# Kernel optimization log

Hardware: AMD Instinct MI355X
Metric: run time of the kernel (lower is better)

## Reference

```python
import jax, jax.numpy as jnp
import numpy as np

OBJ = 6
N_OBJS = 16
ACT = 32
HID = 128


def _mlp(x, W1, b1, W2, b2, W3, b3):
    # RoboticsMLP with layer_sizes=[128,128]: Linear->ReLU->Linear->ReLU->Linear
    h = jax.nn.relu(x @ W1 + b1)
    h = jax.nn.relu(h @ W2 + b2)
    return h @ W3 + b3


def setup_inputs() -> dict:
    key = jax.random.key(0)
    ks = jax.random.split(key, 16)
    B = 4096
    s = lambda fan_in: 1.0 / np.sqrt(fan_in)
    u_in = OBJ + ACT          # 38
    b_in = 2 * OBJ + ACT      # 44
    return {
        "config": jax.random.normal(ks[0], (B, N_OBJS * OBJ), dtype=jnp.float32),
        "action": jax.random.normal(ks[1], (B, ACT), dtype=jnp.float32),
        "uW1": jax.random.normal(ks[2], (u_in, HID), dtype=jnp.float32) * s(u_in),
        "ub1": jnp.zeros((HID,), jnp.float32),
        "uW2": jax.random.normal(ks[3], (HID, HID), dtype=jnp.float32) * s(HID),
        "ub2": jnp.zeros((HID,), jnp.float32),
        "uW3": jax.random.normal(ks[4], (HID, OBJ), dtype=jnp.float32) * s(HID),
        "ub3": jnp.zeros((OBJ,), jnp.float32),
        "bW1": jax.random.normal(ks[5], (b_in, HID), dtype=jnp.float32) * s(b_in),
        "bb1": jnp.zeros((HID,), jnp.float32),
        "bW2": jax.random.normal(ks[6], (HID, HID), dtype=jnp.float32) * s(HID),
        "bb2": jnp.zeros((HID,), jnp.float32),
        "bW3": jax.random.normal(ks[7], (HID, OBJ), dtype=jnp.float32) * s(HID),
        "bb3": jnp.zeros((OBJ,), jnp.float32),
    }


def reference(config, action, uW1, ub1, uW2, ub2, uW3, ub3,
              bW1, bb1, bW2, bb2, bW3, bb3):
    B = config.shape[0]
    objs = config.reshape(B, N_OBJS, OBJ)                       # [B, N, 6]

    # Unary: per-object MLP on [obj, action]
    act_b = jnp.broadcast_to(action[:, None, :], (B, N_OBJS, ACT))
    u_in = jnp.concatenate([objs, act_b], axis=-1)              # [B, N, 6+A]
    u_out = _mlp(u_in, uW1, ub1, uW2, ub2, uW3, ub3)            # [B, N, 6]

    # Binary: all ordered pairs (i, j), i != j: [obj_i, obj_j, action]
    oi = jnp.broadcast_to(objs[:, :, None, :], (B, N_OBJS, N_OBJS, OBJ))
    oj = jnp.broadcast_to(objs[:, None, :, :], (B, N_OBJS, N_OBJS, OBJ))
    act_p = jnp.broadcast_to(action[:, None, None, :], (B, N_OBJS, N_OBJS, ACT))
    b_in = jnp.concatenate([oi, oj, act_p], axis=-1)            # [B, N, N, 12+A]
    b_out = _mlp(b_in, bW1, bb1, bW2, bb2, bW3, bb3)            # [B, N, N, 6]

    # zero out diagonal (i == j skipped in original) then sum over j
    mask = (1.0 - jnp.eye(N_OBJS, dtype=b_out.dtype))[None, :, :, None]
    b_sum = (b_out * mask).sum(axis=2)                          # [B, N, 6]

    out = objs + u_out + b_sum
    return out.reshape(B, N_OBJS * OBJ)
```

## Files before the change

kernel.cpp:

```cpp
#include <hip/hip_runtime.h>

typedef short bf16x8 __attribute__((ext_vector_type(8)));
typedef short bf16x4 __attribute__((ext_vector_type(4)));
typedef float f32x4 __attribute__((ext_vector_type(4)));

__device__ __forceinline__ unsigned short f2bf(float f) {
    unsigned int u = __float_as_uint(f);
    unsigned int r = u + 0x7FFFu + ((u >> 16) & 1u);
    return (unsigned short)(r >> 16);
}

__device__ __forceinline__ unsigned pkbf(float a, float b) {
    unsigned r;
    asm volatile("v_cvt_pk_bf16_f32 %0, %1, %2" : "=v"(r) : "v"(a), "v"(b));
    return r;
}

__device__ __forceinline__ f32x4 mfma16(bf16x4 a, bf16x4 b, f32x4 c) {
#if __has_builtin(__builtin_amdgcn_mfma_f32_16x16x16bf16_1k)
    return __builtin_amdgcn_mfma_f32_16x16x16bf16_1k(a, b, c, 0, 0, 0);
#elif __has_builtin(__builtin_amdgcn_mfma_f32_16x16x16_bf16)
    return __builtin_amdgcn_mfma_f32_16x16x16_bf16(a, b, c, 0, 0, 0);
#else
    asm volatile("v_mfma_f32_16x16x16_bf16 %0, %1, %2, %0" : "+v"(c) : "v"(a), "v"(b));
    return c;
#endif
}

__global__ __launch_bounds__(256) void prep_all(
        const float* __restrict__ uW1, const float* __restrict__ uW2, const float* __restrict__ uW3,
        const float* __restrict__ bW1, const float* __restrict__ bW2, const float* __restrict__ bW3,
        unsigned short* __restrict__ ws) {
    int idx = blockIdx.x * 256 + threadIdx.x;
    if (idx >= 53248) {
        if (idx < 55296) {
            int li = idx - 53248;
            int e = li & 3, l = (li >> 2) & 63, s = li >> 8;
            int k = 16 * s + 4 * (l >> 4) + e, n = l & 15;
            float v = (n < 6) ? bW3[k * 6 + n] : 0.f;
            ws[53248 + li] = f2bf(v);
        }
        return;
    }
    const float* W; int Ksrc, Nsrc, ntsh; unsigned short* dst; int li;
    if (idx < 8192)       { W = uW1; Ksrc = 38;  Nsrc = 128; ntsh = 10; dst = ws;         li = idx; }
    else if (idx < 16384) { W = bW1; Ksrc = 44;  Nsrc = 128; ntsh = 10; dst = ws + 8192;  li = idx - 8192; }
    else if (idx < 32768) { W = uW2; Ksrc = 128; Nsrc = 128; ntsh = 11; dst = ws + 16384; li = idx - 16384; }
    else if (idx < 49152) { W = bW2; Ksrc = 128; Nsrc = 128; ntsh = 11; dst = ws + 32768; li = idx - 32768; }
    else if (idx < 51200) { W = uW3; Ksrc = 128; Nsrc = 6;   ntsh = 11; dst = ws + 49152; li = idx - 49152; }
    else                  { W = bW3; Ksrc = 128; Nsrc = 6;   ntsh = 11; dst = ws + 51200; li = idx - 51200; }
    int e  = li & 7;
    int l  = (li >> 3) & 63;
    int KS = (ntsh == 10) ? 2 : 4;
    int ks = (li >> 9) & (KS - 1);
    int nt = li >> ntsh;
    int k  = ks * 32 + (l >> 4) * 8 + e;
    int n  = nt * 16 + (l & 15);
    float v = (k < Ksrc && n < Nsrc) ? W[k * Nsrc + n] : 0.0f;
    dst[li] = f2bf(v);
}

__global__ __launch_bounds__(256, 3) void unary_kernel(
        const float* __restrict__ config, const float* __restrict__ action,
        const unsigned short* __restrict__ W1f, const float* __restrict__ b1,
        const unsigned short* __restrict__ W2f, const float* __restrict__ b2,
        const unsigned short* __restrict__ W3f, const float* __restrict__ b3,
        float* __restrict__ out) {
    __shared__ __align__(16) unsigned char smem[4 * 8192];
    const int tid = threadIdx.x;
    const int w = tid >> 6;
    const int l = tid & 63;
    const int g = l >> 4;
    const int c = l & 15;
    unsigned char* buf = smem + w * 8192;

    {
        const int rowL = l >> 1;
        const int kh   = l & 1;
        const int sw   = (rowL & 7) << 4;
        const int base = rowL * 128 + kh * 64;
        const int rg = blockIdx.x * 128 + w * 32 + rowL;
        const int b = rg >> 4;
        const int i = rg & 15;
        const float* cbr = config + b * 96 + i * 6;
        const float* ab  = action + b * 32;
        if (kh == 0) {
            float ov[6];
            { const float2 t0 = *(const float2*)(cbr);
              const float2 t1 = *(const float2*)(cbr + 2);
              const float2 t2 = *(const float2*)(cbr + 4);
              ov[0]=t0.x; ov[1]=t0.y; ov[2]=t1.x; ov[3]=t1.y; ov[4]=t2.x; ov[5]=t2.y; }
            float av[26];
            #pragma unroll
            for (int q = 0; q < 6; ++q) {
                const float4 t = *(const float4*)(ab + 4 * q);
                av[4*q]=t.x; av[4*q+1]=t.y; av[4*q+2]=t.z; av[4*q+3]=t.w;
            }
            { const float2 t = *(const float2*)(ab + 24); av[24]=t.x; av[25]=t.y; }
            #pragma unroll
            for (int ch = 0; ch < 4; ++ch) {
                float x[8];
                #pragma unroll
                for (int t8 = 0; t8 < 8; ++t8) {
                    const int k = ch * 8 + t8;
                    x[t8] = (k < 6) ? ov[k] : av[k - 6];
                }
                union { unsigned uu[4]; bf16x8 v; } U;
                U.uu[0] = pkbf(x[0], x[1]); U.uu[1] = pkbf(x[2], x[3]);
                U.uu[2] = pkbf(x[4], x[5]); U.uu[3] = pkbf(x[6], x[7]);
                *(bf16x8*)(buf + ((base + ch * 16) ^ sw)) = U.v;
            }
        } else {
            float av2[6];
            { const float2 t = *(const float2*)(ab + 26); av2[0]=t.x; av2[1]=t.y; }
            { const float4 t = *(const float4*)(ab + 28); av2[2]=t.x; av2[3]=t.y; av2[4]=t.z; av2[5]=t.w; }
            {
                union { unsigned uu[4]; bf16x8 v; } U;
                U.uu[0] = pkbf(av2[0], av2[1]); U.uu[1] = pkbf(av2[2], av2[3]);
                U.uu[2] = pkbf(av2[4], av2[5]); U.uu[3] = 0u;
                *(bf16x8*)(buf + ((base + 0) ^ sw)) = U.v;
            }
            const bf16x8 z = {0,0,0,0,0,0,0,0};
            *(bf16x8*)(buf + ((base + 16) ^ sw)) = z;
            *(bf16x8*)(buf + ((base + 32) ^ sw)) = z;
            *(bf16x8*)(buf + ((base + 48) ^ sw)) = z;
        }
    }
    __syncthreads();

    const f32x4 zero4 = {0.f, 0.f, 0.f, 0.f};

    bf16x8 xf[2][2];
    #pragma unroll
    for (int mt = 0; mt < 2; ++mt)
        #pragma unroll
        for (int ks = 0; ks < 2; ++ks) {
            const int row = mt * 16 + c;
            xf[mt][ks] = *(const bf16x8*)(buf + ((row * 128 + ks * 64 + g * 16) ^ ((c & 7) << 4)));
        }

    #pragma unroll
    for (int nh = 0; nh < 2; ++nh) {
        f32x4 acc[2][4];
        #pragma unroll
        for (int mt = 0; mt < 2; ++mt)
            #pragma unroll
            for (int ntl = 0; ntl < 4; ++ntl) acc[mt][ntl] = zero4;
        #pragma unroll
        for (int ntl = 0; ntl < 4; ++ntl) {
            const int nt = nh * 4 + ntl;
            #pragma unroll
            for (int ks = 0; ks < 2; ++ks) {
                const bf16x8 bfr = *(const bf16x8*)(W1f + ((nt * 2 + ks) * 64 + l) * 8);
                #pragma unroll
                for (int mt = 0; mt < 2; ++mt)
                    acc[mt][ntl] = __builtin_amdgcn_mfma_f32_16x16x32_bf16(xf[mt][ks], bfr, acc[mt][ntl], 0, 0, 0);
            }
        }
        #pragma unroll
        for (int ntl = 0; ntl < 4; ++ntl) {
            const int col = (nh * 4 + ntl) * 16 + c;
            const float bias = b1[col];
            #pragma unroll
            for (int mt = 0; mt < 2; ++mt)
                #pragma unroll
                for (int r = 0; r < 4; ++r) {
                    const int row = mt * 16 + g * 4 + r;
                    const float hv = fmaxf(acc[mt][ntl][r] + bias, 0.f);
                    *(unsigned short*)(buf + ((row * 256 + col * 2) ^ ((row & 7) << 4))) = f2bf(hv);
                }
        }
    }
    __syncthreads();

    bf16x8 hf[2][4];
    #pragma unroll
    for (int mt = 0; mt < 2; ++mt)
        #pragma unroll
        for (int ks = 0; ks < 4; ++ks) {
            const int row = mt * 16 + c;
            hf[mt][ks] = *(const bf16x8*)(buf + ((row * 256 + ks * 64 + g * 16) ^ ((c & 7) << 4)));
        }

    #pragma unroll
    for (int nh = 0; nh < 2; ++nh) {
        f32x4 acc[2][4];
        #pragma unroll
        for (int mt = 0; mt < 2; ++mt)
            #pragma unroll
            for (int ntl = 0; ntl < 4; ++ntl) acc[mt][ntl] = zero4;
        #pragma unroll
        for (int ntl = 0; ntl < 4; ++ntl) {
            const int nt = nh * 4 + ntl;
            #pragma unroll
            for (int ks = 0; ks < 4; ++ks) {
                const bf16x8 bfr = *(const bf16x8*)(W2f + ((nt * 4 + ks) * 64 + l) * 8);
                #pragma unroll
                for (int mt = 0; mt < 2; ++mt)
                    acc[mt][ntl] = __builtin_amdgcn_mfma_f32_16x16x32_bf16(hf[mt][ks], bfr, acc[mt][ntl], 0, 0, 0);
            }
        }
        #pragma unroll
        for (int ntl = 0; ntl < 4; ++ntl) {
            const int col = (nh * 4 + ntl) * 16 + c;
            const float bias = b2[col];
            #pragma unroll
            for (int mt = 0; mt < 2; ++mt)
                #pragma unroll
                for (int r = 0; r < 4; ++r) {
                    const int row = mt * 16 + g * 4 + r;
                    const float hv = fmaxf(acc[mt][ntl][r] + bias, 0.f);
                    *(unsigned short*)(buf + ((row * 256 + col * 2) ^ ((row & 7) << 4))) = f2bf(hv);
                }
        }
    }
    __syncthreads();

    bf16x8 h2f[2][4];
    #pragma unroll
    for (int mt = 0; mt < 2; ++mt)
        #pragma unroll
        for (int ks = 0; ks < 4; ++ks) {
            const int row = mt * 16 + c;
            h2f[mt][ks] = *(const bf16x8*)(buf + ((row * 256 + ks * 64 + g * 16) ^ ((c & 7) << 4)));
        }

    f32x4 acc3[2];
    acc3[0] = zero4; acc3[1] = zero4;
    #pragma unroll
    for (int ks = 0; ks < 4; ++ks) {
        const bf16x8 bfr = *(const bf16x8*)(W3f + (ks * 64 + l) * 8);
        #pragma unroll
        for (int mt = 0; mt < 2; ++mt)
            acc3[mt] = __builtin_amdgcn_mfma_f32_16x16x32_bf16(h2f[mt][ks], bfr, acc3[mt], 0, 0, 0);
    }

    const int rgbase = blockIdx.x * 128 + w * 32;
    const float b3v = (c < 6) ? b3[c] : 0.f;
    #pragma unroll
    for (int mt = 0; mt < 2; ++mt)
        #pragma unroll
        for (int r = 0; r < 4; ++r) {
            const int rg = rgbase + mt * 16 + g * 4 + r;
            const int b = rg >> 4, i = rg & 15;
            if (c < 6) {
                const int idx = b * 96 + i * 6 + c;
                out[idx] = acc3[mt][r] + b3v + config[idx];
            }
        }
}

__global__ __launch_bounds__(256, 4) void binary_kernel(
        const float* __restrict__ config, const float* __restrict__ action,
        const unsigned short* __restrict__ W1f, const float* __restrict__ b1,
        const unsigned short* __restrict__ W2f, const float* __restrict__ b2,
        const unsigned short* __restrict__ W3s, const float* __restrict__ b3,
        float* __restrict__ out) {
    __shared__ __align__(16) unsigned char PQs[12288];

    const int tid = threadIdx.x;
    const int w = tid >> 6, l = tid & 63, g = l >> 4, c = l & 15;
    const int b = blockIdx.x >> 1, h = blockIdx.x & 1;
    const float* cb = config + b * 96;
    const float* ab = action + b * 32;
    const f32x4 zero4 = {0.f, 0.f, 0.f, 0.f};

    bf16x8 wf1[2][2];
    #pragma unroll
    for (int mt1 = 0; mt1 < 2; ++mt1)
        #pragma unroll
        for (int ksp = 0; ksp < 2; ++ksp)
            wf1[mt1][ksp] = *(const bf16x8*)(W1f + (((2 * w + mt1) * 2 + ksp) * 64 + l) * 8);
    f32x4 b1v[2];
    b1v[0] = *(const f32x4*)(b1 + 32 * w + 4 * g);
    b1v[1] = *(const f32x4*)(b1 + 32 * w + 16 + 4 * g);
    const float b3v = (c < 6) ? b3[c] : 0.f;

    bf16x8 tP0, tP1, tQ0;
    {
        const bf16x8 z8 = {0,0,0,0,0,0,0,0};
        tP0 = z8; tP1 = z8; tQ0 = z8;
        union { unsigned u[4]; bf16x8 v; } U;
        if (g == 0) {
            const float* obp = cb + (8 * h + (c & 7)) * 6;
            const float2 a0 = *(const float2*)obp, a1 = *(const float2*)(obp + 2), a2v = *(const float2*)(obp + 4);
            U.u[0] = pkbf(a0.x, a0.y); U.u[1] = pkbf(a1.x, a1.y); U.u[2] = pkbf(a2v.x, a2v.y); U.u[3] = 0u;
            tP0 = U.v;
            const float4 b0 = *(const float4*)(ab + 20), b1q = *(const float4*)(ab + 24);
            U.u[0] = pkbf(b0.x, b0.y); U.u[1] = pkbf(b0.z, b0.w);
            U.u[2] = pkbf(b1q.x, b1q.y); U.u[3] = pkbf(b1q.z, b1q.w);
            tP1 = U.v;
            const float2 q0 = *(const float2*)(cb + c * 6);
            U.u[0] = 0u; U.u[1] = 0u; U.u[2] = 0u; U.u[3] = pkbf(q0.x, q0.y);
            tQ0 = U.v;
        } else if (g == 1) {
            const float4 b0 = *(const float4*)(ab + 0);
            U.u[0] = 0u; U.u[1] = 0u; U.u[2] = pkbf(b0.x, b0.y); U.u[3] = pkbf(b0.z, b0.w);
            tP0 = U.v;
            const float4 b1q = *(const float4*)(ab + 28);
            U.u[0] = pkbf(b1q.x, b1q.y); U.u[1] = pkbf(b1q.z, b1q.w); U.u[2] = 0u; U.u[3] = 0u;
            tP1 = U.v;
            const float* obq = cb + c * 6;
            const float2 q1 = *(const float2*)(obq + 2), q2 = *(const float2*)(obq + 4);
            U.u[0] = pkbf(q1.x, q1.y); U.u[1] = pkbf(q2.x, q2.y); U.u[2] = 0u; U.u[3] = 0u;
            tQ0 = U.v;
        } else if (g == 2) {
            const float4 b0 = *(const float4*)(ab + 4), b1q = *(const float4*)(ab + 8);
            U.u[0] = pkbf(b0.x, b0.y); U.u[1] = pkbf(b0.z, b0.w);
            U.u[2] = pkbf(b1q.x, b1q.y); U.u[3] = pkbf(b1q.z, b1q.w);
            tP0 = U.v;
        } else {
            const float4 b0 = *(const float4*)(ab + 12), b1q = *(const float4*)(ab + 16);
            U.u[0] = pkbf(b0.x, b0.y); U.u[1] = pkbf(b0.z, b0.w);
            U.u[2] = pkbf(b1q.x, b1q.y); U.u[3] = pkbf(b1q.z, b1q.w);
            tP0 = U.v;
        }
    }

    {
        f32x4 acc1[2][2];
        acc1[0][0] = b1v[0]; acc1[0][1] = zero4;
        acc1[1][0] = b1v[1]; acc1[1][1] = zero4;
        #pragma unroll
        for (int mt1 = 0; mt1 < 2; ++mt1) {
            acc1[mt1][0] = __builtin_amdgcn_mfma_f32_16x16x32_bf16(wf1[mt1][0], tP0, acc1[mt1][0], 0, 0, 0);
            acc1[mt1][0] = __builtin_amdgcn_mfma_f32_16x16x32_bf16(wf1[mt1][1], tP1, acc1[mt1][0], 0, 0, 0);
            acc1[mt1][1] = __builtin_amdgcn_mfma_f32_16x16x32_bf16(wf1[mt1][0], tQ0, acc1[mt1][1], 0, 0, 0);
        }
        #pragma unroll
        for (int mt1 = 0; mt1 < 2; ++mt1) {
            const int fb = (32 * w + 16 * mt1 + 4 * g) * 4;
            if (c < 8) {
                float2 v0; v0.x = acc1[mt1][0][0]; v0.y = acc1[mt1][0][1];
                float2 v1; v1.x = acc1[mt1][0][2]; v1.y = acc1[mt1][0][3];
                *(float2*)(PQs + ((c * 512 + fb)     ^ ((c & 7) << 4))) = v0;
                *(float2*)(PQs + ((c * 512 + fb + 8) ^ ((c & 7) << 4))) = v1;
            }
            {
                const int row = 8 + c;
                float2 v0; v0.x = acc1[mt1][1][0]; v0.y = acc1[mt1][1][1];
                float2 v1; v1.x = acc1[mt1][1][2]; v1.y = acc1[mt1][1][3];
                *(float2*)(PQs + ((row * 512 + fb)     ^ ((c & 7) << 4))) = v0;
                *(float2*)(PQs + ((row * 512 + fb + 8) ^ ((c & 7) << 4))) = v1;
            }
        }
    }
    __syncthreads();

    const int i0 = h * 8 + 2 * w;
    bf16x8 h1f[2][4];
    #pragma unroll
    for (int ks = 0; ks < 4; ++ks) {
        const int kb = (32 * ks + 8 * g) * 4;
        const f32x4 q0 = *(const f32x4*)(PQs + (((8 + c) * 512 + kb) ^ ((c & 7) << 4)));
        const f32x4 q1 = *(const f32x4*)(PQs + (((8 + c) * 512 + kb + 16) ^ ((c & 7) << 4)));
        #pragma unroll
        for (int nt = 0; nt < 2; ++nt) {
            const int ip = 2 * w + nt;
            const f32x4 p0 = *(const f32x4*)(PQs + ((ip * 512 + kb) ^ ((ip & 7) << 4)));
            const f32x4 p1 = *(const f32x4*)(PQs + ((ip * 512 + kb + 16) ^ ((ip & 7) << 4)));
            union { unsigned u[4]; bf16x8 v; } un;
            un.u[0] = pkbf(fmaxf(p0[0] + q0[0], 0.f), fmaxf(p0[1] + q0[1], 0.f));
            un.u[1] = pkbf(fmaxf(p0[2] + q0[2], 0.f), fmaxf(p0[3] + q0[3], 0.f));
            un.u[2] = pkbf(fmaxf(p1[0] + q1[0], 0.f), fmaxf(p1[1] + q1[1], 0.f));
            un.u[3] = pkbf(fmaxf(p1[2] + q1[2], 0.f), fmaxf(p1[3] + q1[3], 0.f));
            h1f[nt][ks] = un.v;
        }
    }

    f32x4 acc3[2];
    acc3[0][0] = b3v; acc3[0][1] = b3v; acc3[0][2] = b3v; acc3[0][3] = b3v;
    acc3[1] = acc3[0];
    #pragma unroll
    for (int ks = 0; ks < 4; ++ks) {
        bf16x8 wfa[8];
        #pragma unroll
        for (int q = 0; q < 8; ++q)
            wfa[q] = *(const bf16x8*)(W2f + (((2 * ks + (q >> 2)) * 4 + (q & 3)) * 64 + l) * 8);
        union { uint2 u2; bf16x4 v; } w3b[2];
        w3b[0].u2 = *(const uint2*)(W3s + ((2 * ks)     * 64 + l) * 4);
        w3b[1].u2 = *(const uint2*)(W3s + ((2 * ks + 1) * 64 + l) * 4);
        const f32x4 bv0 = *(const f32x4*)(b2 + 32 * ks + 4 * g);
        const f32x4 bv1 = *(const f32x4*)(b2 + 32 * ks + 16 + 4 * g);
        __builtin_amdgcn_sched_barrier(0);

        f32x4 a2[2][2];
        a2[0][0] = bv0; a2[0][1] = bv0;
        a2[1][0] = bv1; a2[1][1] = bv1;
        #pragma unroll
        for (int ksp = 0; ksp < 4; ++ksp) {
            #pragma unroll
            for (int mt1 = 0; mt1 < 2; ++mt1) {
                a2[mt1][0] = __builtin_amdgcn_mfma_f32_16x16x32_bf16(wfa[mt1 * 4 + ksp], h1f[0][ksp], a2[mt1][0], 0, 0, 0);
                a2[mt1][1] = __builtin_amdgcn_mfma_f32_16x16x32_bf16(wfa[mt1 * 4 + ksp], h1f[1][ksp], a2[mt1][1], 0, 0, 0);
            }
        }
        #pragma unroll
        for (int mt1 = 0; mt1 < 2; ++mt1) {
            #pragma unroll
            for (int nt = 0; nt < 2; ++nt) {
                union { unsigned u[2]; bf16x4 v; } pa;
                pa.u[0] = pkbf(fmaxf(a2[mt1][nt][0], 0.f), fmaxf(a2[mt1][nt][1], 0.f));
                pa.u[1] = pkbf(fmaxf(a2[mt1][nt][2], 0.f), fmaxf(a2[mt1][nt][3], 0.f));
                acc3[nt] = mfma16(pa.v, w3b[mt1].v, acc3[nt]);
            }
        }
    }

    #pragma unroll
    for (int nt = 0; nt < 2; ++nt) {
        const int i = i0 + nt;
        float s = 0.f;
        #pragma unroll
        for (int r = 0; r < 4; ++r) {
            const int j = 4 * g + r;
            if (j != i) s += acc3[nt][r];
        }
        s += __shfl_xor(s, 16, 64);
        s += __shfl_xor(s, 32, 64);
        if (g == 0 && c < 6) out[b * 96 + i * 6 + c] += s;
    }
}

extern "C" void kernel_launch(void* const* d_in, const int* in_sizes, int n_in,
                              void* d_out, int out_size, void* d_ws, size_t ws_size,
                              hipStream_t stream) {
    const float* config = (const float*)d_in[0];
    const float* action = (const float*)d_in[1];
    const float* uW1 = (const float*)d_in[2];
    const float* ub1 = (const float*)d_in[3];
    const float* uW2 = (const float*)d_in[4];
    const float* ub2 = (const float*)d_in[5];
    const float* uW3 = (const float*)d_in[6];
    const float* ub3 = (const float*)d_in[7];
    const float* bW1 = (const float*)d_in[8];
    const float* bb1 = (const float*)d_in[9];
    const float* bW2 = (const float*)d_in[10];
    const float* bb2 = (const float*)d_in[11];
    const float* bW3 = (const float*)d_in[12];
    const float* bb3 = (const float*)d_in[13];
    float* out = (float*)d_out;

    unsigned short* ws   = (unsigned short*)d_ws;
    unsigned short* uW1f = ws;
    unsigned short* bW1f = ws + 8192;
    unsigned short* uW2f = ws + 16384;
    unsigned short* bW2f = ws + 32768;
    unsigned short* uW3f = ws + 49152;
    unsigned short* bW3s = ws + 53248;

    prep_all<<<216, 256, 0, stream>>>(uW1, uW2, uW3, bW1, bW2, bW3, ws);
    unary_kernel<<<512, 256, 0, stream>>>(config, action, uW1f, ub1, uW2f, ub2, uW3f, ub3, out);
    binary_kernel<<<8192, 256, 0, stream>>>(config, action, bW1f, bb1, bW2f, bb2, bW3s, bb3, out);
}
```

Measured before the change: 162.7 us.

## Fuse unary and binary MLPs into one kernel, one block per batch

Merges the unary and binary kernels into a single kernel where each block handles one batch element and all 16 objects, instead of two blocks per batch. The binary layer-2 weights are staged in LDS once per block, and the unary MLP reuses the same first-layer object/action fragments via a reordered uW1 layout. This removes the read-modify-write of the output, the separate unary launch and duplicated input loads. In exchange it uses more LDS and registers, dropping occupancy to 2 blocks per CU.

```diff
diff --git a/kernel.cpp b/kernel.cpp
--- a/kernel.cpp
+++ b/kernel.cpp
@@ -32,249 +32,75 @@
         const float* __restrict__ bW1, const float* __restrict__ bW2, const float* __restrict__ bW3,
         unsigned short* __restrict__ ws) {
     int idx = blockIdx.x * 256 + threadIdx.x;
-    if (idx >= 53248) {
-        if (idx < 55296) {
-            int li = idx - 53248;
-            int e = li & 3, l = (li >> 2) & 63, s = li >> 8;
-            int k = 16 * s + 4 * (l >> 4) + e, n = l & 15;
-            float v = (n < 6) ? bW3[k * 6 + n] : 0.f;
-            ws[53248 + li] = f2bf(v);
-        }
+    if (idx >= 53248) return;
+    if (idx >= 49152) {
+        const float* W = (idx < 51200) ? bW3 : uW3;
+        int li = (idx - 49152) & 2047;
+        int e = li & 3, l = (li >> 2) & 63, s = li >> 8;
+        int k = 16 * s + 4 * (l >> 4) + e, n = l & 15;
+        ws[idx] = f2bf((n < 6) ? W[k * 6 + n] : 0.f);
         return;
     }
-    const float* W; int Ksrc, Nsrc, ntsh; unsigned short* dst; int li;
-    if (idx < 8192)       { W = uW1; Ksrc = 38;  Nsrc = 128; ntsh = 10; dst = ws;         li = idx; }
-    else if (idx < 16384) { W = bW1; Ksrc = 44;  Nsrc = 128; ntsh = 10; dst = ws + 8192;  li = idx - 8192; }
-    else if (idx < 32768) { W = uW2; Ksrc = 128; Nsrc = 128; ntsh = 11; dst = ws + 16384; li = idx - 16384; }
-    else if (idx < 49152) { W = bW2; Ksrc = 128; Nsrc = 128; ntsh = 11; dst = ws + 32768; li = idx - 32768; }
-    else if (idx < 51200) { W = uW3; Ksrc = 128; Nsrc = 6;   ntsh = 11; dst = ws + 49152; li = idx - 49152; }
-    else                  { W = bW3; Ksrc = 128; Nsrc = 6;   ntsh = 11; dst = ws + 51200; li = idx - 51200; }
-    int e  = li & 7;
-    int l  = (li >> 3) & 63;
-    int KS = (ntsh == 10) ? 2 : 4;
+    int seg, li; const float* W; int KS;
+    if (idx < 8192)       { seg = 0; li = idx;         W = bW1; KS = 2; }
+    else if (idx < 16384) { seg = 1; li = idx - 8192;  W = uW1; KS = 2; }
+    else if (idx < 32768) { seg = 2; li = idx - 16384; W = bW2; KS = 4; }
+    else                  { seg = 3; li = idx - 32768; W = uW2; KS = 4; }
+    int e = li & 7, l = (li >> 3) & 63;
     int ks = (li >> 9) & (KS - 1);
-    int nt = li >> ntsh;
-    int k  = ks * 32 + (l >> 4) * 8 + e;
-    int n  = nt * 16 + (l & 15);
-    float v = (k < Ksrc && n < Nsrc) ? W[k * Nsrc + n] : 0.0f;
-    dst[li] = f2bf(v);
-}
-
-__global__ __launch_bounds__(256, 3) void unary_kernel(
+    int nt = li >> ((KS == 2) ? 10 : 11);
+    int k = 32 * ks + 8 * (l >> 4) + e;
+    int n = 16 * nt + (l & 15);
+    float v;
+    if (seg == 0)      v = (k < 44) ? W[k * 128 + n] : 0.f;
+    else if (seg == 1) { int ksrc = (k < 6) ? k : (k >= 12 && k < 44) ? (k - 6) : -1;
+                         v = (ksrc >= 0) ? W[ksrc * 128 + n] : 0.f; }
+    else               v = W[k * 128 + n];
+    ws[idx] = f2bf(v);
+}
+
+__global__ __launch_bounds__(256, 2) void fused_kernel(
         const float* __restrict__ config, const float* __restrict__ action,
-        const unsigned short* __restrict__ W1f, const float* __restrict__ b1,
-        const unsigned short* __restrict__ W2f, const float* __restrict__ b2,
-        const unsigned short* __restrict__ W3f, const float* __restrict__ b3,
+        const unsigned short* __restrict__ bW1f, const float* __restrict__ bb1,
+        const unsigned short* __restrict__ uW1f, const float* __restrict__ ub1,
+        const unsigned short* __restrict__ bW2f, const float* __restrict__ bb2,
+        const unsigned short* __restrict__ uW2f, const float* __restrict__ ub2,
+        const unsigned short* __restrict__ bW3s, const float* __restrict__ bb3,
+        const unsigned short* __restrict__ uW3s, const float* __restrict__ ub3,
         float* __restrict__ out) {
-    __shared__ __align__(16) unsigned char smem[4 * 8192];
-    const int tid = threadIdx.x;
-    const int w = tid >> 6;
-    const int l = tid & 63;
-    const int g = l >> 4;
-    const int c = l & 15;
-    unsigned char* buf = smem + w * 8192;
-
-    {
-        const int rowL = l >> 1;
-        const int kh   = l & 1;
-        const int sw   = (rowL & 7) << 4;
-        const int base = rowL * 128 + kh * 64;
-        const int rg = blockIdx.x * 128 + w * 32 + rowL;
-        const int b = rg >> 4;
-        const int i = rg & 15;
-        const float* cbr = config + b * 96 + i * 6;
-        const float* ab  = action + b * 32;
-        if (kh == 0) {
-            float ov[6];
-            { const float2 t0 = *(const float2*)(cbr);
-              const float2 t1 = *(const float2*)(cbr + 2);
-              const float2 t2 = *(const float2*)(cbr + 4);
-              ov[0]=t0.x; ov[1]=t0.y; ov[2]=t1.x; ov[3]=t1.y; ov[4]=t2.x; ov[5]=t2.y; }
-            float av[26];
-            #pragma unroll
-            for (int q = 0; q < 6; ++q) {
-                const float4 t = *(const float4*)(ab + 4 * q);
-                av[4*q]=t.x; av[4*q+1]=t.y; av[4*q+2]=t.z; av[4*q+3]=t.w;
-            }
-            { const float2 t = *(const float2*)(ab + 24); av[24]=t.x; av[25]=t.y; }
-            #pragma unroll
-            for (int ch = 0; ch < 4; ++ch) {
-                float x[8];
-                #pragma unroll
-                for (int t8 = 0; t8 < 8; ++t8) {
-                    const int k = ch * 8 + t8;
-                    x[t8] = (k < 6) ? ov[k] : av[k - 6];
-                }
-                union { unsigned uu[4]; bf16x8 v; } U;
-                U.uu[0] = pkbf(x[0], x[1]); U.uu[1] = pkbf(x[2], x[3]);
-                U.uu[2] = pkbf(x[4], x[5]); U.uu[3] = pkbf(x[6], x[7]);
-                *(bf16x8*)(buf + ((base + ch * 16) ^ sw)) = U.v;
-            }
-        } else {
-            float av2[6];
-            { const float2 t = *(const float2*)(ab + 26); av2[0]=t.x; av2[1]=t.y; }
-            { const float4 t = *(const float4*)(ab + 28); av2[2]=t.x; av2[3]=t.y; av2[4]=t.z; av2[5]=t.w; }
-            {
-                union { unsigned uu[4]; bf16x8 v; } U;
-                U.uu[0] = pkbf(av2[0], av2[1]); U.uu[1] = pkbf(av2[2], av2[3]);
-                U.uu[2] = pkbf(av2[4], av2[5]); U.uu[3] = 0u;
-                *(bf16x8*)(buf + ((base + 0) ^ sw)) = U.v;
-            }
-            const bf16x8 z = {0,0,0,0,0,0,0,0};
-            *(bf16x8*)(buf + ((base + 16) ^ sw)) = z;
-            *(bf16x8*)(buf + ((base + 32) ^ sw)) = z;
-            *(bf16x8*)(buf + ((base + 48) ^ sw)) = z;
-        }
-    }
-    __syncthreads();
-
-    const f32x4 zero4 = {0.f, 0.f, 0.f, 0.f};
-
-    bf16x8 xf[2][2];
-    #pragma unroll
-    for (int mt = 0; mt < 2; ++mt)
-        #pragma unroll
-        for (int ks = 0; ks < 2; ++ks) {
-            const int row = mt * 16 + c;
-            xf[mt][ks] = *(const bf16x8*)(buf + ((row * 128 + ks * 64 + g * 16) ^ ((c & 7) << 4)));
-        }
-
-    #pragma unroll
-    for (int nh = 0; nh < 2; ++nh) {
-        f32x4 acc[2][4];
-        #pragma unroll
-        for (int mt = 0; mt < 2; ++mt)
-            #pragma unroll
-            for (int ntl = 0; ntl < 4; ++ntl) acc[mt][ntl] = zero4;
-        #pragma unroll
-        for (int ntl = 0; ntl < 4; ++ntl) {
-            const int nt = nh * 4 + ntl;
-            #pragma unroll
-            for (int ks = 0; ks < 2; ++ks) {
-                const bf16x8 bfr = *(const bf16x8*)(W1f + ((nt * 2 + ks) * 64 + l) * 8);
-                #pragma unroll
-                for (int mt = 0; mt < 2; ++mt)
-                    acc[mt][ntl] = __builtin_amdgcn_mfma_f32_16x16x32_bf16(xf[mt][ks], bfr, acc[mt][ntl], 0, 0, 0);
-            }
-        }
-        #pragma unroll
-        for (int ntl = 0; ntl < 4; ++ntl) {
-            const int col = (nh * 4 + ntl) * 16 + c;
-            const float bias = b1[col];
-            #pragma unroll
-            for (int mt = 0; mt < 2; ++mt)
-                #pragma unroll
-                for (int r = 0; r < 4; ++r) {
-                    const int row = mt * 16 + g * 4 + r;
-                    const float hv = fmaxf(acc[mt][ntl][r] + bias, 0.f);
-                    *(unsigned short*)(buf + ((row * 256 + col * 2) ^ ((row & 7) << 4))) = f2bf(hv);
-                }
-        }
-    }
-    __syncthreads();
-
-    bf16x8 hf[2][4];
-    #pragma unroll
-    for (int mt = 0; mt < 2; ++mt)
-        #pragma unroll
-        for (int ks = 0; ks < 4; ++ks) {
-            const int row = mt * 16 + c;
-            hf[mt][ks] = *(const bf16x8*)(buf + ((row * 256 + ks * 64 + g * 16) ^ ((c & 7) << 4)));
-        }
-
-    #pragma unroll
-    for (int nh = 0; nh < 2; ++nh) {
-        f32x4 acc[2][4];
-        #pragma unroll
-        for (int mt = 0; mt < 2; ++mt)
-            #pragma unroll
-            for (int ntl = 0; ntl < 4; ++ntl) acc[mt][ntl] = zero4;
-        #pragma unroll
-        for (int ntl = 0; ntl < 4; ++ntl) {
-            const int nt = nh * 4 + ntl;
-            #pragma unroll
-            for (int ks = 0; ks < 4; ++ks) {
-                const bf16x8 bfr = *(const bf16x8*)(W2f + ((nt * 4 + ks) * 64 + l) * 8);
-                #pragma unroll
-                for (int mt = 0; mt < 2; ++mt)
-                    acc[mt][ntl] = __builtin_amdgcn_mfma_f32_16x16x32_bf16(hf[mt][ks], bfr, acc[mt][ntl], 0, 0, 0);
-            }
-        }
-        #pragma unroll
-        for (int ntl = 0; ntl < 4; ++ntl) {
-            const int col = (nh * 4 + ntl) * 16 + c;
-            const float bias = b2[col];
-            #pragma unroll
-            for (int mt = 0; mt < 2; ++mt)
-                #pragma unroll
-                for (int r = 0; r < 4; ++r) {
-                    const int row = mt * 16 + g * 4 + r;
-                    const float hv = fmaxf(acc[mt][ntl][r] + bias, 0.f);
-                    *(unsigned short*)(buf + ((row * 256 + col * 2) ^ ((row & 7) << 4))) = f2bf(hv);
-                }
-        }
-    }
-    __syncthreads();
-
-    bf16x8 h2f[2][4];
-    #pragma unroll
-    for (int mt = 0; mt < 2; ++mt)
-        #pragma unroll
-        for (int ks = 0; ks < 4; ++ks) {
-            const int row = mt * 16 + c;
-            h2f[mt][ks] = *(const bf16x8*)(buf + ((row * 256 + ks * 64 + g * 16) ^ ((c & 7) << 4)));
-        }
-
-    f32x4 acc3[2];
-    acc3[0] = zero4; acc3[1] = zero4;
-    #pragma unroll
-    for (int ks = 0; ks < 4; ++ks) {
-        const bf16x8 bfr = *(const bf16x8*)(W3f + (ks * 64 + l) * 8);
-        #pragma unroll
-        for (int mt = 0; mt < 2; ++mt)
-            acc3[mt] = __builtin_amdgcn_mfma_f32_16x16x32_bf16(h2f[mt][ks], bfr, acc3[mt], 0, 0, 0);
-    }
-
-    const int rgbase = blockIdx.x * 128 + w * 32;
-    const float b3v = (c < 6) ? b3[c] : 0.f;
-    #pragma unroll
-    for (int mt = 0; mt < 2; ++mt)
-        #pragma unroll
-        for (int r = 0; r < 4; ++r) {
-            const int rg = rgbase + mt * 16 + g * 4 + r;
-            const int b = rg >> 4, i = rg & 15;
-            if (c < 6) {
-                const int idx = b * 96 + i * 6 + c;
-                out[idx] = acc3[mt][r] + b3v + config[idx];
-            }
-        }
-}
-
-__global__ __launch_bounds__(256, 4) void binary_kernel(
-        const float* __restrict__ config, const float* __restrict__ action,
-        const unsigned short* __restrict__ W1f, const float* __restrict__ b1,
-        const unsigned short* __restrict__ W2f, const float* __restrict__ b2,
-        const unsigned short* __restrict__ W3s, const float* __restrict__ b3,
-        float* __restrict__ out) {
-    __shared__ __align__(16) unsigned char PQs[12288];
+    __shared__ __align__(16) unsigned char PQs[16384];
+    __shared__ __align__(16) unsigned char Pus[8192];
+    __shared__ __align__(16) unsigned char W2s[32768];
+    __shared__ __align__(16) float Psum[1024];
 
     const int tid = threadIdx.x;
     const int w = tid >> 6, l = tid & 63, g = l >> 4, c = l & 15;
-    const int b = blockIdx.x >> 1, h = blockIdx.x & 1;
+    const int b = blockIdx.x;
     const float* cb = config + b * 96;
     const float* ab = action + b * 32;
     const f32x4 zero4 = {0.f, 0.f, 0.f, 0.f};
 
-    bf16x8 wf1[2][2];
+    uint4 stg[8];
+    {
+        const uint4* s4 = (const uint4*)bW2f;
+        #pragma unroll
+        for (int it = 0; it < 8; ++it) stg[it] = s4[tid + 256 * it];
+    }
+
+    bf16x8 wfb[2][2], wfu[2][2];
     #pragma unroll
     for (int mt1 = 0; mt1 < 2; ++mt1)
         #pragma unroll
-        for (int ksp = 0; ksp < 2; ++ksp)
-            wf1[mt1][ksp] = *(const bf16x8*)(W1f + (((2 * w + mt1) * 2 + ksp) * 64 + l) * 8);
-    f32x4 b1v[2];
-    b1v[0] = *(const f32x4*)(b1 + 32 * w + 4 * g);
-    b1v[1] = *(const f32x4*)(b1 + 32 * w + 16 + 4 * g);
-    const float b3v = (c < 6) ? b3[c] : 0.f;
+        for (int ksp = 0; ksp < 2; ++ksp) {
+            wfb[mt1][ksp] = *(const bf16x8*)(bW1f + (((2 * w + mt1) * 2 + ksp) * 64 + l) * 8);
+            wfu[mt1][ksp] = *(const bf16x8*)(uW1f + (((2 * w + mt1) * 2 + ksp) * 64 + l) * 8);
+        }
+    f32x4 b1v[2], ub1v[2];
+    b1v[0]  = *(const f32x4*)(bb1 + 32 * w + 4 * g);
+    b1v[1]  = *(const f32x4*)(bb1 + 32 * w + 16 + 4 * g);
+    ub1v[0] = *(const f32x4*)(ub1 + 32 * w + 4 * g);
+    ub1v[1] = *(const f32x4*)(ub1 + 32 * w + 16 + 4 * g);
+    const float b3v = (c < 6) ? bb3[c] : 0.f;
 
     bf16x8 tP0, tP1, tQ0;
     {
@@ -282,7 +108,7 @@
         tP0 = z8; tP1 = z8; tQ0 = z8;
         union { unsigned u[4]; bf16x8 v; } U;
         if (g == 0) {
-            const float* obp = cb + (8 * h + (c & 7)) * 6;
+            const float* obp = cb + c * 6;
             const float2 a0 = *(const float2*)obp, a1 = *(const float2*)(obp + 2), a2v = *(const float2*)(obp + 4);
             U.u[0] = pkbf(a0.x, a0.y); U.u[1] = pkbf(a1.x, a1.y); U.u[2] = pkbf(a2v.x, a2v.y); U.u[3] = 0u;
             tP0 = U.v;
@@ -290,8 +116,7 @@
             U.u[0] = pkbf(b0.x, b0.y); U.u[1] = pkbf(b0.z, b0.w);
             U.u[2] = pkbf(b1q.x, b1q.y); U.u[3] = pkbf(b1q.z, b1q.w);
             tP1 = U.v;
-            const float2 q0 = *(const float2*)(cb + c * 6);
-            U.u[0] = 0u; U.u[1] = 0u; U.u[2] = 0u; U.u[3] = pkbf(q0.x, q0.y);
+            U.u[0] = 0u; U.u[1] = 0u; U.u[2] = 0u; U.u[3] = pkbf(a0.x, a0.y);
             tQ0 = U.v;
         } else if (g == 1) {
             const float4 b0 = *(const float4*)(ab + 0);
@@ -318,98 +143,146 @@
     }
 
     {
-        f32x4 acc1[2][2];
+        f32x4 acc1[2][2], accu[2];
         acc1[0][0] = b1v[0]; acc1[0][1] = zero4;
         acc1[1][0] = b1v[1]; acc1[1][1] = zero4;
+        accu[0] = ub1v[0]; accu[1] = ub1v[1];
         #pragma unroll
         for (int mt1 = 0; mt1 < 2; ++mt1) {
-            acc1[mt1][0] = __builtin_amdgcn_mfma_f32_16x16x32_bf16(wf1[mt1][0], tP0, acc1[mt1][0], 0, 0, 0);
-            acc1[mt1][0] = __builtin_amdgcn_mfma_f32_16x16x32_bf16(wf1[mt1][1], tP1, acc1[mt1][0], 0, 0, 0);
-            acc1[mt1][1] = __builtin_amdgcn_mfma_f32_16x16x32_bf16(wf1[mt1][0], tQ0, acc1[mt1][1], 0, 0, 0);
-        }
+            acc1[mt1][0] = __builtin_amdgcn_mfma_f32_16x16x32_bf16(wfb[mt1][0], tP0, acc1[mt1][0], 0, 0, 0);
+            acc1[mt1][0] = __builtin_amdgcn_mfma_f32_16x16x32_bf16(wfb[mt1][1], tP1, acc1[mt1][0], 0, 0, 0);
+            acc1[mt1][1] = __builtin_amdgcn_mfma_f32_16x16x32_bf16(wfb[mt1][0], tQ0, acc1[mt1][1], 0, 0, 0);
+            accu[mt1]    = __builtin_amdgcn_mfma_f32_16x16x32_bf16(wfu[mt1][0], tP0, accu[mt1], 0, 0, 0);
+            accu[mt1]    = __builtin_amdgcn_mfma_f32_16x16x32_bf16(wfu[mt1][1], tP1, accu[mt1], 0, 0, 0);
+        }
+        const int sw = (c & 7) << 4;
         #pragma unroll
         for (int mt1 = 0; mt1 < 2; ++mt1) {
             const int fb = (32 * w + 16 * mt1 + 4 * g) * 4;
-            if (c < 8) {
+            {
                 float2 v0; v0.x = acc1[mt1][0][0]; v0.y = acc1[mt1][0][1];
                 float2 v1; v1.x = acc1[mt1][0][2]; v1.y = acc1[mt1][0][3];
-                *(float2*)(PQs + ((c * 512 + fb)     ^ ((c & 7) << 4))) = v0;
-                *(float2*)(PQs + ((c * 512 + fb + 8) ^ ((c & 7) << 4))) = v1;
+                *(float2*)(PQs + ((c * 512 + fb)     ^ sw)) = v0;
+                *(float2*)(PQs + ((c * 512 + fb + 8) ^ sw)) = v1;
             }
             {
-                const int row = 8 + c;
                 float2 v0; v0.x = acc1[mt1][1][0]; v0.y = acc1[mt1][1][1];
                 float2 v1; v1.x = acc1[mt1][1][2]; v1.y = acc1[mt1][1][3];
-                *(float2*)(PQs + ((row * 512 + fb)     ^ ((c & 7) << 4))) = v0;
-                *(float2*)(PQs + ((row * 512 + fb + 8) ^ ((c & 7) << 4))) = v1;
-            }
-        }
+                *(float2*)(PQs + (((16 + c) * 512 + fb)     ^ sw)) = v0;
+                *(float2*)(PQs + (((16 + c) * 512 + fb + 8) ^ sw)) = v1;
+            }
+            {
+                float2 v0; v0.x = accu[mt1][0]; v0.y = accu[mt1][1];
+                float2 v1; v1.x = accu[mt1][2]; v1.y = accu[mt1][3];
+                *(float2*)(Pus + ((c * 512 + fb)     ^ sw)) = v0;
+                *(float2*)(Pus + ((c * 512 + fb + 8) ^ sw)) = v1;
+            }
+        }
+    }
+    {
+        #pragma unroll
+        for (int it = 0; it < 8; ++it)
+            *(uint4*)(W2s + tid * 16 + it * 4096) = stg[it];
     }
     __syncthreads();
 
-    const int i0 = h * 8 + 2 * w;
-    bf16x8 h1f[2][4];
+    bf16x8 h1f[4][4], h1uf[4];
+    {
+        const int sw_c = (c & 7) << 4;
+        #pragma unroll
+        for (int ks = 0; ks < 4; ++ks) {
+            const int kb = (32 * ks + 8 * g) * 4;
+            const f32x4 q0 = *(const f32x4*)(PQs + (((16 + c) * 512 + kb)      ^ sw_c));
+            const f32x4 q1 = *(const f32x4*)(PQs + (((16 + c) * 512 + kb + 16) ^ sw_c));
+            const f32x4 u0 = *(const f32x4*)(Pus + ((c * 512 + kb)      ^ sw_c));
+            const f32x4 u1 = *(const f32x4*)(Pus + ((c * 512 + kb + 16) ^ sw_c));
+            union { unsigned u[4]; bf16x8 v; } uu;
+            uu.u[0] = pkbf(fmaxf(u0[0], 0.f), fmaxf(u0[1], 0.f));
+            uu.u[1] = pkbf(fmaxf(u0[2], 0.f), fmaxf(u0[3], 0.f));
+            uu.u[2] = pkbf(fmaxf(u1[0], 0.f), fmaxf(u1[1], 0.f));
+            uu.u[3] = pkbf(fmaxf(u1[2], 0.f), fmaxf(u1[3], 0.f));
+            h1uf[ks] = uu.v;
+            #pragma unroll
+            for (int nt = 0; nt < 4; ++nt) {
+                const int ip = 4 * w + nt;
+                const f32x4 p0 = *(const f32x4*)(PQs + ((ip * 512 + kb)      ^ ((ip & 7) << 4)));
+                const f32x4 p1 = *(const f32x4*)(PQs + ((ip * 512 + kb + 16) ^ ((ip & 7) << 4)));
+                union { unsigned u[4]; bf16x8 v; } un;
+                un.u[0] = pkbf(fmaxf(p0[0] + q0[0], 0.f), fmaxf(p0[1] + q0[1], 0.f));
+                un.u[1] = pkbf(fmaxf(p0[2] + q0[2], 0.f), fmaxf(p0[3] + q0[3], 0.f));
+                un.u[2] = pkbf(fmaxf(p1[0] + q1[0], 0.f), fmaxf(p1[1] + q1[1], 0.f));
+                un.u[3] = pkbf(fmaxf(p1[2] + q1[2], 0.f), fmaxf(p1[3] + q1[3], 0.f));
+                h1f[nt][ks] = un.v;
+            }
+        }
+    }
+
+    f32x4 acc3[4];
     #pragma unroll
-    for (int ks = 0; ks < 4; ++ks) {
-        const int kb = (32 * ks + 8 * g) * 4;
-        const f32x4 q0 = *(const f32x4*)(PQs + (((8 + c) * 512 + kb) ^ ((c & 7) << 4)));
-        const f32x4 q1 = *(const f32x4*)(PQs + (((8 + c) * 512 + kb + 16) ^ ((c & 7) << 4)));
-        #pragma unroll
-        for (int nt = 0; nt < 2; ++nt) {
-            const int ip = 2 * w + nt;
-            const f32x4 p0 = *(const f32x4*)(PQs + ((ip * 512 + kb) ^ ((ip & 7) << 4)));
-            const f32x4 p1 = *(const f32x4*)(PQs + ((ip * 512 + kb + 16) ^ ((ip & 7) << 4)));
-            union { unsigned u[4]; bf16x8 v; } un;
-            un.u[0] = pkbf(fmaxf(p0[0] + q0[0], 0.f), fmaxf(p0[1] + q0[1], 0.f));
-            un.u[1] = pkbf(fmaxf(p0[2] + q0[2], 0.f), fmaxf(p0[3] + q0[3], 0.f));
-            un.u[2] = pkbf(fmaxf(p1[0] + q1[0], 0.f), fmaxf(p1[1] + q1[1], 0.f));
-            un.u[3] = pkbf(fmaxf(p1[2] + q1[2], 0.f), fmaxf(p1[3] + q1[3], 0.f));
-            h1f[nt][ks] = un.v;
-        }
-    }
-
-    f32x4 acc3[2];
-    acc3[0][0] = b3v; acc3[0][1] = b3v; acc3[0][2] = b3v; acc3[0][3] = b3v;
-    acc3[1] = acc3[0];
+    for (int nt = 0; nt < 4; ++nt) { acc3[nt][0] = b3v; acc3[nt][1] = b3v; acc3[nt][2] = b3v; acc3[nt][3] = b3v; }
     #pragma unroll
     for (int ks = 0; ks < 4; ++ks) {
         bf16x8 wfa[8];
         #pragma unroll
         for (int q = 0; q < 8; ++q)
-            wfa[q] = *(const bf16x8*)(W2f + (((2 * ks + (q >> 2)) * 4 + (q & 3)) * 64 + l) * 8);
+            wfa[q] = *(const bf16x8*)(W2s + ((2 * ks + (q >> 2)) * 4 + (q & 3)) * 1024 + l * 16);
         union { uint2 u2; bf16x4 v; } w3b[2];
-        w3b[0].u2 = *(const uint2*)(W3s + ((2 * ks)     * 64 + l) * 4);
-        w3b[1].u2 = *(const uint2*)(W3s + ((2 * ks + 1) * 64 + l) * 4);
-        const f32x4 bv0 = *(const f32x4*)(b2 + 32 * ks + 4 * g);
-        const f32x4 bv1 = *(const f32x4*)(b2 + 32 * ks + 16 + 4 * g);
-        __builtin_amdgcn_sched_barrier(0);
-
-        f32x4 a2[2][2];
-        a2[0][0] = bv0; a2[0][1] = bv0;
-        a2[1][0] = bv1; a2[1][1] = bv1;
-        #pragma unroll
-        for (int ksp = 0; ksp < 4; ++ksp) {
+        w3b[0].u2 = *(const uint2*)(bW3s + ((2 * ks)     * 64 + l) * 4);
+        w3b[1].u2 = *(const uint2*)(bW3s + ((2 * ks + 1) * 64 + l) * 4);
+        const f32x4 bv0 = *(const f32x4*)(bb2 + 32 * ks + 4 * g);
+        const f32x4 bv1 = *(const f32x4*)(bb2 + 32 * ks + 16 + 4 * g);
+
+        f32x4 a2[2][4];
+        #pragma unroll
+        for (int nt = 0; nt < 4; ++nt) { a2[0][nt] = bv0; a2[1][nt] = bv1; }
+        #pragma unroll
+        for (int ksp = 0; ksp < 4; ++ksp)
             #pragma unroll
-            for (int mt1 = 0; mt1 < 2; ++mt1) {
-                a2[mt1][0] = __builtin_amdgcn_mfma_f32_16x16x32_bf16(wfa[mt1 * 4 + ksp], h1f[0][ksp], a2[mt1][0], 0, 0, 0);
-                a2[mt1][1] = __builtin_amdgcn_mfma_f32_16x16x32_bf16(wfa[mt1 * 4 + ksp], h1f[1][ksp], a2[mt1][1], 0, 0, 0);
-            }
-        }
-        #pragma unroll
-        for (int mt1 = 0; mt1 < 2; ++mt1) {
+            for (int mt1 = 0; mt1 < 2; ++mt1)
+                #pragma unroll
+                for (int nt = 0; nt < 4; ++nt)
+                    a2[mt1][nt] = __builtin_amdgcn_mfma_f32_16x16x32_bf16(wfa[mt1 * 4 + ksp], h1f[nt][ksp], a2[mt1][nt], 0, 0, 0);
+        #pragma unroll
+        for (int mt1 = 0; mt1 < 2; ++mt1)
             #pragma unroll
-            for (int nt = 0; nt < 2; ++nt) {
+            for (int nt = 0; nt < 4; ++nt) {
                 union { unsigned u[2]; bf16x4 v; } pa;
                 pa.u[0] = pkbf(fmaxf(a2[mt1][nt][0], 0.f), fmaxf(a2[mt1][nt][1], 0.f));
                 pa.u[1] = pkbf(fmaxf(a2[mt1][nt][2], 0.f), fmaxf(a2[mt1][nt][3], 0.f));
                 acc3[nt] = mfma16(pa.v, w3b[mt1].v, acc3[nt]);
             }
-        }
-    }
+    }
+
+    {
+        f32x4 a2u[2];
+        a2u[0] = *(const f32x4*)(ub2 + 32 * w + 4 * g);
+        a2u[1] = *(const f32x4*)(ub2 + 32 * w + 16 + 4 * g);
+        #pragma unroll
+        for (int ksp = 0; ksp < 4; ++ksp)
+            #pragma unroll
+            for (int mt1 = 0; mt1 < 2; ++mt1) {
+                const bf16x8 wf = *(const bf16x8*)(uW2f + (((2 * w + mt1) * 4 + ksp) * 64 + l) * 8);
+                a2u[mt1] = __builtin_amdgcn_mfma_f32_16x16x32_bf16(wf, h1uf[ksp], a2u[mt1], 0, 0, 0);
+            }
+        f32x4 acc3u = zero4;
+        #pragma unroll
+        for (int mt1 = 0; mt1 < 2; ++mt1) {
+            union { uint2 u2; bf16x4 v; } w3u;
+            w3u.u2 = *(const uint2*)(uW3s + ((2 * w + mt1) * 64 + l) * 4);
+            union { unsigned u[2]; bf16x4 v; } pa;
+            pa.u[0] = pkbf(fmaxf(a2u[mt1][0], 0.f), fmaxf(a2u[mt1][1], 0.f));
+            pa.u[1] = pkbf(fmaxf(a2u[mt1][2], 0.f), fmaxf(a2u[mt1][3], 0.f));
+            acc3u = mfma16(pa.v, w3u.v, acc3u);
+        }
+        #pragma unroll
+        for (int r = 0; r < 4; ++r)
+            Psum[w * 256 + (4 * g + r) * 16 + c] = acc3u[r];
+    }
+    __syncthreads();
 
     #pragma unroll
-    for (int nt = 0; nt < 2; ++nt) {
-        const int i = i0 + nt;
+    for (int nt = 0; nt < 4; ++nt) {
+        const int i = 4 * w + nt;
         float s = 0.f;
         #pragma unroll
         for (int r = 0; r < 4; ++r) {
@@ -418,7 +291,11 @@
         }
         s += __shfl_xor(s, 16, 64);
         s += __shfl_xor(s, 32, 64);
-        if (g == 0 && c < 6) out[b * 96 + i * 6 + c] += s;
+        if (g == 0 && c < 6) {
+            const float u = Psum[i * 16 + c] + Psum[256 + i * 16 + c]
+                          + Psum[512 + i * 16 + c] + Psum[768 + i * 16 + c];
+            out[b * 96 + i * 6 + c] = u + ub3[c] + cb[i * 6 + c] + s;
+        }
     }
 }
 
@@ -441,15 +318,17 @@
     const float* bb3 = (const float*)d_in[13];
     float* out = (float*)d_out;
 
-    unsigned short* ws   = (unsigned short*)d_ws;
-    unsigned short* uW1f = ws;
-    unsigned short* bW1f = ws + 8192;
-    unsigned short* uW2f = ws + 16384;
-    unsigned short* bW2f = ws + 32768;
-    unsigned short* uW3f = ws + 49152;
-    unsigned short* bW3s = ws + 53248;
-
-    prep_all<<<216, 256, 0, stream>>>(uW1, uW2, uW3, bW1, bW2, bW3, ws);
-    unary_kernel<<<512, 256, 0, stream>>>(config, action, uW1f, ub1, uW2f, ub2, uW3f, ub3, out);
-    binary_kernel<<<8192, 256, 0, stream>>>(config, action, bW1f, bb1, bW2f, bb2, bW3s, bb3, out);
-}
+    unsigned short* ws    = (unsigned short*)d_ws;
+    unsigned short* bW1f  = ws;
+    unsigned short* uW1f  = ws + 8192;
+    unsigned short* bW2f  = ws + 16384;
+    unsigned short* uW2f  = ws + 32768;
+    unsigned short* bW3s  = ws + 49152;
+    unsigned short* uW3s  = ws + 51200;
+
+    prep_all<<<208, 256, 0, stream>>>(uW1, uW2, uW3, bW1, bW2, bW3, ws);
+    fused_kernel<<<4096, 256, 0, stream>>>(config, action,
+                                           bW1f, bb1, uW1f, ub1,
+                                           bW2f, bb2, uW2f, ub2,
+                                           bW3s, bb3, uW3s, ub3, out);
+}
```

Result: faster. 148.8 us (-8.6%).
